# Kernel optimization log

Hardware: AMD Instinct MI355X
Metric: run time of the kernel (lower is better)

Reference implementation:

```python
import jax, jax.numpy as jnp
import numpy as np

N = 10000          # nodes
E = 320000         # edges
C = 128            # num_features (channels per irrep)
RB = 8             # radial basis size
NS = 10            # num_species
HID = 64           # radial MLP hidden
NPATH = 5          # TP paths: 0x0->0, 0x1->1, 1x0->1, 1x1->0(dot), 1x1->1(cross)
EPS = 0.17677669529663687  # 1/sqrt(avg_degree=32)


def setup_inputs() -> dict:
    key = jax.random.key(0)
    ks = jax.random.split(key, 20)
    inp = {
        "vectors": jax.random.normal(ks[0], (E, 3), jnp.float32),
        "node_feats": jax.random.normal(ks[1], (N, C * 4), jnp.float32),
        "node_specie": jax.random.randint(ks[2], (N,), 0, NS),
        "radial_embedding": jax.random.normal(ks[3], (E, RB), jnp.float32),
        "senders": jax.random.randint(ks[4], (E,), 0, N),
        "receivers": jax.random.randint(ks[5], (E,), 0, N),
    }
    s = 1.0 / np.sqrt(C)
    inp["W_up_s"] = jax.random.normal(ks[6], (C, C), jnp.float32) * s
    inp["W_up_v"] = jax.random.normal(ks[7], (C, C), jnp.float32) * s
    inp["W_rad1"] = jax.random.normal(ks[8], (RB, HID), jnp.float32) / np.sqrt(RB)
    inp["W_rad2"] = jax.random.normal(ks[9], (HID, NPATH * C), jnp.float32) / np.sqrt(HID)
    inp["W_down_s"] = jax.random.normal(ks[10], (C, C), jnp.float32) * s
    inp["W_down_v"] = jax.random.normal(ks[11], (C, C), jnp.float32) * s
    inp["W_skip_s"] = jax.random.normal(ks[12], (NS, C, C), jnp.float32) * s
    inp["W_skip_v"] = jax.random.normal(ks[13], (NS, C, C), jnp.float32) * s
    inp["W_prod_s"] = jax.random.normal(ks[14], (NS, 3, C), jnp.float32)
    inp["W_prod_v"] = jax.random.normal(ks[15], (NS, 2, C), jnp.float32)
    inp["W_lin_s"] = jax.random.normal(ks[16], (C, C), jnp.float32) * s
    inp["W_lin_v"] = jax.random.normal(ks[17], (C, C), jnp.float32) * s
    inp["W_ro"] = jax.random.normal(ks[18], (C, 1), jnp.float32) * s
    return inp


def _mace_forward(vectors, node_feats, node_specie, radial_embedding, senders,
                  receivers, W_up_s, W_up_v, W_rad1, W_rad2, W_down_s, W_down_v,
                  W_skip_s, W_skip_v, W_prod_s, W_prod_v, W_lin_s, W_lin_v, W_ro):
    n = node_feats.shape[0]
    # split flat mul_ir layout: [C x 0e | C x 1o]
    s = node_feats[:, :C]                      # [N, C]
    v = node_feats[:, C:].reshape(n, C, 3)     # [N, C, 3]

    # --- skip connection (species-indexed linear, first=False) ---
    Ws = W_skip_s[node_specie]                 # [N, C, C]
    Wv = W_skip_v[node_specie]
    sc_s = jnp.einsum('nc,ncd->nd', s, Ws)
    sc_v = jnp.einsum('nci,ncd->ndi', v, Wv)

    # --- interaction: linear_up ---
    h_s = s @ W_up_s
    h_v = jnp.einsum('nci,cd->ndi', v, W_up_v)

    # spherical harmonics (component normalization): Y1 = sqrt(3)*r_hat
    norm = jnp.linalg.norm(vectors, axis=-1, keepdims=True)
    Y1 = jnp.sqrt(3.0) * vectors / (norm + 1e-9)           # [E, 3]

    # radial MLP -> per-edge, per-path, per-channel TP weights
    w = jax.nn.silu(radial_embedding @ W_rad1) @ W_rad2
    w = w.reshape(-1, NPATH, C)                            # [E, 5, C]

    # gather sender features, depthwise ('uvu') CG tensor product with Y
    s_j = h_s[senders]                                     # [E, C]
    v_j = h_v[senders]                                     # [E, C, 3]
    dot = jnp.einsum('eci,ei->ec', v_j, Y1)                # 1o x 1o -> 0e
    crs = jnp.cross(v_j, Y1[:, None, :])                   # 1o x 1o -> 1o
    m_s = w[:, 0] * s_j + w[:, 3] * dot                    # [E, C]
    m_v = (w[:, 1][:, :, None] * s_j[:, :, None] * Y1[:, None, :]
           + w[:, 2][:, :, None] * v_j
           + w[:, 4][:, :, None] * crs)                    # [E, C, 3]

    # scatter to receivers
    agg_s = jax.ops.segment_sum(m_s, receivers, num_segments=n)
    agg_v = jax.ops.segment_sum(m_v, receivers, num_segments=n)

    # linear_down + epsilon scaling
    f_s = (agg_s @ W_down_s) * EPS
    f_v = jnp.einsum('nci,cd->ndi', agg_v, W_down_v) * EPS

    # --- equivariant product basis (correlation=2, symmetric) ---
    # order-1 and order-2 symmetric contractions for (0e, 1o) inputs:
    # scalars: A_s, A_s^2, |A_v|^2 ; vectors: A_v, A_s * A_v
    B_s = jnp.stack([f_s, f_s * f_s, jnp.sum(f_v * f_v, axis=-1)], axis=1)  # [N,3,C]
    B_v = jnp.stack([f_v, f_s[:, :, None] * f_v], axis=1)                    # [N,2,C,3]
    p_s = jnp.einsum('nkc,nkc->nc', B_s, W_prod_s[node_specie])
    p_v = jnp.einsum('nkci,nkc->nci', B_v, W_prod_v[node_specie])
    out_s = p_s @ W_lin_s + sc_s
    out_v = jnp.einsum('nci,cd->ndi', p_v, W_lin_v) + sc_v

    # --- linear readout (not last layer): invariant 0e output ---
    node_outputs = out_s @ W_ro                            # [N, 1]
    new_feats = jnp.concatenate([out_s, out_v.reshape(n, C * 3)], axis=-1)
    return node_outputs, new_feats


def reference(vectors, node_feats, node_specie, radial_embedding, senders,
              receivers, W_up_s, W_up_v, W_rad1, W_rad2, W_down_s, W_down_v,
              W_skip_s, W_skip_v, W_prod_s, W_prod_v, W_lin_s, W_lin_v, W_ro):
    return _mace_forward(vectors, node_feats, node_specie, radial_embedding,
                         senders, receivers, W_up_s, W_up_v, W_rad1, W_rad2,
                         W_down_s, W_down_v, W_skip_s, W_skip_v, W_prod_s,
                         W_prod_v, W_lin_s, W_lin_v, W_ro)
```

## Files before the change

### kernel.cpp

```cpp
#include <hip/hip_runtime.h>
#include <hip/hip_bf16.h>


#define NN 10000
#define EE 320000
#define FEPS 0.17677669529663687f

typedef __attribute__((ext_vector_type(4))) float f32x4;
typedef __attribute__((ext_vector_type(8))) short s16x8;

__device__ __forceinline__ float bflo(unsigned u) { return __uint_as_float(u << 16); }
__device__ __forceinline__ float bfhi(unsigned u) { return __uint_as_float(u & 0xffff0000u); }
__device__ __forceinline__ unsigned short f2bu(float f) {
    unsigned u = __float_as_uint(f);
    return (unsigned short)((u + 0x7FFFu + ((u >> 16) & 1u)) >> 16);
}
__device__ __forceinline__ unsigned pack2(float a, float b) {
    return (unsigned)f2bu(a) | ((unsigned)f2bu(b) << 16);
}
__device__ __forceinline__ s16x8 pack8(float4 a, float4 b) {
    union { s16x8 v; unsigned short u[8]; } r;
    r.u[0] = f2bu(a.x); r.u[1] = f2bu(a.y); r.u[2] = f2bu(a.z); r.u[3] = f2bu(a.w);
    r.u[4] = f2bu(b.x); r.u[5] = f2bu(b.y); r.u[6] = f2bu(b.z); r.u[7] = f2bu(b.w);
    return r.v;
}

#define TWN (26 * 16384)
#define W2N (640 * 64)
#define PREPX 20
#define HISTB 1250
__global__ __launch_bounds__(256) void k_prep_hist(
    const float* __restrict__ Wus, const float* __restrict__ Wuv,
    const float* __restrict__ Wds, const float* __restrict__ Wdv,
    const float* __restrict__ Wls, const float* __restrict__ Wlv,
    const float* __restrict__ Wss, const float* __restrict__ Wsv,
    const float* __restrict__ W_rad2,
    unsigned short* __restrict__ T,
    unsigned short* __restrict__ w2t,
    const int* __restrict__ recv, int* __restrict__ cnt) {
    const int b = blockIdx.x, tid = threadIdx.x;
    if (b < 26) {
        __shared__ unsigned short tr[128][130];
        const int m = b;
        const float* src;
        if (m == 0) src = Wus; else if (m == 1) src = Wuv;
        else if (m == 2) src = Wds; else if (m == 3) src = Wdv;
        else if (m == 4) src = Wls; else if (m == 5) src = Wlv;
        else if (m < 16) src = Wss + (size_t)(m - 6) * 16384;
        else src = Wsv + (size_t)(m - 16) * 16384;
        for (int i = tid; i < 16384; i += 256) {
            const int c = i >> 7, d = i & 127;
            tr[d][c] = f2bu(src[i]);
        }
        __syncthreads();
        unsigned* o32 = (unsigned*)(T + (size_t)m * 16384);
        for (int i = tid; i < 8192; i += 256) {
            const int d = i >> 6, c2 = (i & 63) * 2;
            o32[i] = (unsigned)tr[d][c2] | ((unsigned)tr[d][c2 + 1] << 16);
        }
    } else if (b < 26 + PREPX) {
        for (int i = (b - 26) * 256 + tid; i < W2N; i += PREPX * 256) {
            const int n = i >> 6, k = i & 63;
            w2t[i] = f2bu(W_rad2[k * 640 + n]);
        }
    } else {
        const int e = (b - (26 + PREPX)) * 256 + tid;
        if (e < EE) {
            int r = recv[e];
            r = ((unsigned)r < NN) ? r : 0;
            atomicAdd(&cnt[r], 1);
        }
    }
}

__global__ __launch_bounds__(1024) void k_scan_spec(
    const int* __restrict__ cnt, int* __restrict__ offs, int* __restrict__ cur,
    const int* __restrict__ specie, int* __restrict__ perm,
    int2* __restrict__ tiles, int* __restrict__ ntiles) {
    __shared__ int sums[1024];
    __shared__ int hcnt[10], hbase[10], hcur[10], tbase[11];
    const int t = threadIdx.x;
    const int chunk = (NN + 1023) / 1024;
    const int start = t * chunk;
    int local = 0;
    for (int i = 0; i < chunk; i++) {
        int idx = start + i;
        if (idx < NN) local += cnt[idx];
    }
    sums[t] = local;
    __syncthreads();
    for (int ofs = 1; ofs < 1024; ofs <<= 1) {
        int u = (t >= ofs) ? sums[t - ofs] : 0;
        __syncthreads();
        sums[t] += u;
        __syncthreads();
    }
    int base = (t == 0) ? 0 : sums[t - 1];
    for (int i = 0; i < chunk; i++) {
        int idx = start + i;
        if (idx < NN) {
            offs[idx] = base;
            cur[idx] = base;
            base += cnt[idx];
        }
    }
    if (t == 0) offs[NN] = sums[1023];
    if (t < 10) hcnt[t] = 0;
    __syncthreads();
    for (int n = t; n < NN; n += 1024) {
        int s = specie[n];
        s = ((unsigned)s < 10) ? s : 0;
        atomicAdd(&hcnt[s], 1);
    }
    __syncthreads();
    if (t == 0) {
        int run = 0, tc = 0;
        for (int sp = 0; sp < 10; sp++) {
            hbase[sp] = run; hcur[sp] = run; run += hcnt[sp];
            tbase[sp] = tc;  tc += (hcnt[sp] + 15) >> 4;
        }
        tbase[10] = tc;
        *ntiles = tc;
    }
    __syncthreads();
    const int tc = tbase[10];
    for (int ti = t; ti < tc; ti += 1024) {
        int sp = 0;
        while (sp < 9 && ti >= tbase[sp + 1]) sp++;
        const int b = (ti - tbase[sp]) * 16;
        tiles[ti] = make_int2(hbase[sp] + b, (sp << 8) | min(16, hcnt[sp] - b));
    }
    for (int n = t; n < NN; n += 1024) {
        int s = specie[n];
        s = ((unsigned)s < 10) ? s : 0;
        int slot = atomicAdd(&hcur[s], 1);
        if ((unsigned)slot < NN) perm[slot] = n;
    }
}

__global__ __launch_bounds__(256) void k_fill_pre(
    const int* __restrict__ recv, int* __restrict__ cur, int* __restrict__ csr,
    const float* __restrict__ nf,
    const unsigned short* __restrict__ Tw,
    uint2* __restrict__ h4o,
    const int* __restrict__ perm, const int2* __restrict__ tiles,
    const int* __restrict__ ntiles,
    float4* __restrict__ sc4) {
    if (blockIdx.x >= 640) {
        const int e = (blockIdx.x - 640) * 256 + threadIdx.x;
        if (e < EE) {
            int r = recv[e];
            r = ((unsigned)r < NN) ? r : 0;
            int slot = atomicAdd(&cur[r], 1);
            if ((unsigned)slot < EE) csr[slot] = e;
        }
        return;
    }
    const int tile = blockIdx.x;
    if (tile >= *ntiles) return;
    const int2 td = tiles[tile];
    const int base = td.x, sp = td.y >> 8, cnt16 = td.y & 255;
    __shared__ int nodesl[16];
    __shared__ float nfl[16][512];
    const int tid = threadIdx.x;
    if (tid < 16) nodesl[tid] = perm[base + ((tid < cnt16) ? tid : 0)];
    __syncthreads();
    {
        float4* dst = (float4*)nfl;
        for (int i = tid; i < 2048; i += 256) {
            const int r = i >> 7, off = i & 127;
            dst[i] = ((const float4*)(nf + (size_t)nodesl[r] * 512))[off];
        }
    }
    __syncthreads();
    const int lane = tid & 63, wv = tid >> 6;
    const int col = lane & 15, quad = lane >> 4;
    const float* rp = nfl[col];
    s16x8 Af[4][4];
#pragma unroll
    for (int kt = 0; kt < 4; kt++) {
        const int ko = kt * 32 + quad * 8;
        const float4 fa = *(const float4*)(rp + ko);
        const float4 fb = *(const float4*)(rp + ko + 4);
        Af[0][kt] = pack8(fa, fb);
#pragma unroll
        for (int i = 0; i < 3; i++) {
            union { s16x8 v; unsigned short u[8]; } A;
#pragma unroll
            for (int j = 0; j < 8; j++) A.u[j] = f2bu(rp[128 + 3 * (ko + j) + i]);
            Af[1 + i][kt] = A.v;
        }
    }
    const unsigned short* Ts = Tw;
    const unsigned short* Tv = Tw + 16384;
    const unsigned short* Tss = Tw + (size_t)(6 + sp) * 16384;
    const unsigned short* Tsv = Tw + (size_t)(16 + sp) * 16384;
#pragma unroll
    for (int nt = 0; nt < 2; nt++) {
        const int d = 32 * wv + 16 * nt + col;
        f32x4 C[4];
#pragma unroll
        for (int m = 0; m < 4; m++) C[m] = (f32x4){0.f, 0.f, 0.f, 0.f};
#pragma unroll
        for (int kt = 0; kt < 4; kt++) {
            const int ko = kt * 32 + quad * 8;
            const s16x8 Bs = *(const s16x8*)&Ts[(size_t)d * 128 + ko];
            const s16x8 Bv = *(const s16x8*)&Tv[(size_t)d * 128 + ko];
            C[0] = __builtin_amdgcn_mfma_f32_16x16x32_bf16(Af[0][kt], Bs, C[0], 0, 0, 0);
#pragma unroll
            for (int i = 0; i < 3; i++)
                C[1 + i] = __builtin_amdgcn_mfma_f32_16x16x32_bf16(Af[1 + i][kt], Bv, C[1 + i], 0, 0, 0);
        }
        const int P = ((d >> 5) << 4) + (d & 15);
        const int half = (d >> 4) & 1;
#pragma unroll
        for (int reg = 0; reg < 4; reg++) {
            const int node = nodesl[quad * 4 + reg];
            h4o[((size_t)node * 64 + P) * 2 + half] =
                make_uint2(pack2(C[0][reg], C[1][reg]), pack2(C[2][reg], C[3][reg]));
        }
        f32x4 CS[4];
#pragma unroll
        for (int m = 0; m < 4; m++) CS[m] = (f32x4){0.f, 0.f, 0.f, 0.f};
#pragma unroll
        for (int kt = 0; kt < 4; kt++) {
            const int ko = kt * 32 + quad * 8;
            const s16x8 Bss = *(const s16x8*)&Tss[(size_t)d * 128 + ko];
            const s16x8 Bsv = *(const s16x8*)&Tsv[(size_t)d * 128 + ko];
            CS[0] = __builtin_amdgcn_mfma_f32_16x16x32_bf16(Af[0][kt], Bss, CS[0], 0, 0, 0);
#pragma unroll
            for (int i = 0; i < 3; i++)
                CS[1 + i] = __builtin_amdgcn_mfma_f32_16x16x32_bf16(Af[1 + i][kt], Bsv, CS[1 + i], 0, 0, 0);
        }
#pragma unroll
        for (int reg = 0; reg < 4; reg++) {
            const int node = nodesl[quad * 4 + reg];
            sc4[(size_t)node * 128 + d] =
                make_float4(CS[0][reg], CS[1][reg], CS[2][reg], CS[3][reg]);
        }
    }
}

#define EGRID 2560
__global__ __launch_bounds__(256, 2) void k_edge_mfma(
    const float* __restrict__ vectors,
    const float* __restrict__ radial,
    const int* __restrict__ senders,
    const float* __restrict__ W_rad1,
    const unsigned short* __restrict__ w2t,
    const uint4* __restrict__ h4q,
    const int* __restrict__ offs, const int* __restrict__ csr,
    unsigned short* __restrict__ aggb) {
    __shared__ unsigned short w1s[512];
    __shared__ float4 em[3][64];
    __shared__ float radl[3][64][8];
    __shared__ unsigned short hidb[2 * 64 * 72];
    const int tid = threadIdx.x;
    const int lane = tid & 63, wv = tid >> 6;
    const int row = lane & 15, quad = lane >> 4;
    const int sE = tid >> 2, st = tid & 3;
    for (int i = tid; i < 512; i += 256) w1s[i] = f2bu(W_rad1[i]);

    s16x8 Bf[2][5][2];
#pragma unroll
    for (int ti = 0; ti < 2; ti++) {
        const int t = 2 * wv + ti;
#pragma unroll
        for (int p = 0; p < 5; p++) {
            const unsigned short* bp =
                w2t + (size_t)(128 * p + 16 * t + row) * 64 + quad * 8;
            Bf[ti][p][0] = *(const s16x8*)(bp);
            Bf[ti][p][1] = *(const s16x8*)(bp + 32);
        }
    }

    int curN = blockIdx.x, curS = offs[curN], curD = offs[curN + 1] - curS, curC0 = 0;
    int nxtN = curN, nxtS = curS, nxtD = curD, nxtC0 = 0;
    {
        nxtC0 += 64;
        if (nxtC0 >= nxtD) {
            nxtN += EGRID;
            if (nxtN < NN) { nxtS = offs[nxtN]; nxtD = offs[nxtN + 1] - nxtS; }
            nxtC0 = 0;
        }
    }
    int nx2N = nxtN, nx2S = nxtS, nx2D = nxtD, nx2C0 = nxtC0;
    if (nx2N < NN) {
        nx2C0 += 64;
        if (nx2C0 >= nx2D) {
            nx2N += EGRID;
            if (nx2N < NN) { nx2S = offs[nx2N]; nx2D = offs[nx2N + 1] - nx2S; }
            nx2C0 = 0;
        }
    }

    if (st < 2) {
        const int gi = curC0 + sE;
        if (gi < curD) {
            int e = csr[curS + gi];
            e = ((unsigned)e < EE) ? e : 0;
            if (st == 0) {
                int j = senders[e];
                j = ((unsigned)j < NN) ? j : 0;
                const float vx = vectors[e * 3 + 0];
                const float vy = vectors[e * 3 + 1];
                const float vz = vectors[e * 3 + 2];
                const float inr = 1.7320508075688772f /
                    (sqrtf(vx * vx + vy * vy + vz * vz) + 1e-9f);
                em[0][sE] = make_float4(__int_as_float(j), vx * inr, vy * inr, vz * inr);
            } else {
                *(float4*)&radl[0][sE][0] = *(const float4*)(radial + (size_t)e * 8);
                *(float4*)&radl[0][sE][4] = *(const float4*)(radial + (size_t)e * 8 + 4);
            }
        } else {
            if (st == 0) em[0][sE] = make_float4(0.f, 0.f, 0.f, 0.f);
            else {
                *(float4*)&radl[0][sE][0] = make_float4(0.f, 0.f, 0.f, 0.f);
                *(float4*)&radl[0][sE][4] = make_float4(0.f, 0.f, 0.f, 0.f);
            }
        }
    }
    int eReg = -1;
    if (nxtN < NN && st < 2) {
        const int gi = nxtC0 + sE;
        if (gi < nxtD) {
            int e = csr[nxtS + gi];
            eReg = ((unsigned)e < EE) ? e : 0;
        }
    }
    __syncthreads();

    float acc_s[2] = {0.f, 0.f}, av0[2] = {0.f, 0.f},
          av1[2] = {0.f, 0.f}, av2[2] = {0.f, 0.f};
    int cs = 0, hbI = 0;
    while (true) {
        const int ws = (cs == 2) ? 0 : cs + 1;
        const bool hasNxt = (nxtN < NN);
        const float4* emc = em[cs];
        const float* emf = (const float*)emc;
        uint4 hqA[4];
#pragma unroll
        for (int rg = 0; rg < 4; rg++) {
            const int j = __float_as_int(emf[(quad * 4 + rg) * 4]);
            hqA[rg] = h4q[(size_t)j * 64 + (wv << 4) + row];
        }
        bool sv = false;
        float4 ra0 = make_float4(0.f, 0.f, 0.f, 0.f);
        float4 ra1 = make_float4(0.f, 0.f, 0.f, 0.f);
        if (hasNxt && st < 2 && eReg >= 0) {
            sv = true;
            const int e = eReg;
            if (st == 0) {
                int j = senders[e];
                j = ((unsigned)j < NN) ? j : 0;
                ra0 = make_float4(vectors[e * 3 + 0], vectors[e * 3 + 1],
                                  vectors[e * 3 + 2], __int_as_float(j));
            } else {
                ra0 = *(const float4*)(radial + (size_t)e * 8);
                ra1 = *(const float4*)(radial + (size_t)e * 8 + 4);
            }
        }
        int eRegN = -1;
        if (nx2N < NN && st < 2) {
            const int gi = nx2C0 + sE;
            if (gi < nx2D) {
                int e = csr[nx2S + gi];
                eRegN = ((unsigned)e < EE) ? e : 0;
            }
        }
        const int glimC = min(64, curD - curC0);
        {
            const int g16C = (glimC + 15) & ~15;
            unsigned short* hb = hidb + hbI * 4608;
            const int u0 = st * 16;
            if (sE < glimC) {
                float rr[8];
                *(float4*)&rr[0] = *(const float4*)&radl[cs][sE][0];
                *(float4*)&rr[4] = *(const float4*)&radl[cs][sE][4];
#pragma unroll
                for (int h = 0; h < 2; h++) {
                    float a[8];
#pragma unroll
                    for (int u = 0; u < 8; u++) a[u] = 0.f;
#pragma unroll
                    for (int r = 0; r < 8; r++) {
                        const uint4 wa = *(const uint4*)&w1s[r * 64 + u0 + h * 8];
                        const float f = rr[r];
                        a[0] += f * bflo(wa.x); a[1] += f * bfhi(wa.x);
                        a[2] += f * bflo(wa.y); a[3] += f * bfhi(wa.y);
                        a[4] += f * bflo(wa.z); a[5] += f * bfhi(wa.z);
                        a[6] += f * bflo(wa.w); a[7] += f * bfhi(wa.w);
                    }
                    unsigned o[4];
#pragma unroll
                    for (int k = 0; k < 4; k++) {
                        const float s0 = a[2 * k] / (1.f + __expf(-a[2 * k]));
                        const float s1 = a[2 * k + 1] / (1.f + __expf(-a[2 * k + 1]));
                        o[k] = pack2(s0, s1);
                    }
                    *(uint4*)&hb[sE * 72 + u0 + h * 8] = make_uint4(o[0], o[1], o[2], o[3]);
                }
            } else if (sE < g16C) {
                *(uint4*)&hb[sE * 72 + u0] = make_uint4(0, 0, 0, 0);
                *(uint4*)&hb[sE * 72 + u0 + 8] = make_uint4(0, 0, 0, 0);
            }
        }
        if (hasNxt && st < 2) {
            if (st == 0) {
                if (sv) {
                    const float vx = ra0.x, vy = ra0.y, vz = ra0.z;
                    const float inr = 1.7320508075688772f /
                        (sqrtf(vx * vx + vy * vy + vz * vz) + 1e-9f);
                    em[ws][sE] = make_float4(ra0.w, vx * inr, vy * inr, vz * inr);
                } else {
                    em[ws][sE] = make_float4(0.f, 0.f, 0.f, 0.f);
                }
            } else {
                *(float4*)&radl[ws][sE][0] = ra0;
                *(float4*)&radl[ws][sE][4] = ra1;
            }
        }
        __syncthreads();
        {
            __builtin_amdgcn_s_setprio(1);
            const unsigned short* hb = hidb + hbI * 4608;
            for (int g0 = 0; g0 < glimC; g0 += 16) {
                const s16x8 A0 = *(const s16x8*)&hb[(g0 + row) * 72 + quad * 8];
                const s16x8 A1 = *(const s16x8*)&hb[(g0 + row) * 72 + 32 + quad * 8];
                float4 mm[4];
#pragma unroll
                for (int rg = 0; rg < 4; rg++) mm[rg] = emc[g0 + quad * 4 + rg];
                const bool more = (g0 + 16) < glimC;
                uint4 hqB[4];
                if (more) {
#pragma unroll
                    for (int rg = 0; rg < 4; rg++) {
                        const int j = __float_as_int(emf[(g0 + 16 + quad * 4 + rg) * 4]);
                        hqB[rg] = h4q[(size_t)j * 64 + (wv << 4) + row];
                    }
                }
#pragma unroll
                for (int ti = 0; ti < 2; ti++) {
                    float sj[4], a0r[4], a1r[4], a2r[4];
#pragma unroll
                    for (int rg = 0; rg < 4; rg++) {
                        const unsigned wx = ti ? hqA[rg].z : hqA[rg].x;
                        const unsigned wy = ti ? hqA[rg].w : hqA[rg].y;
                        sj[rg] = bflo(wx); a0r[rg] = bfhi(wx);
                        a1r[rg] = bflo(wy); a2r[rg] = bfhi(wy);
                    }
#pragma unroll
                    for (int p = 0; p < 5; p++) {
                        f32x4 z = {0.f, 0.f, 0.f, 0.f};
                        z = __builtin_amdgcn_mfma_f32_16x16x32_bf16(A0, Bf[ti][p][0], z, 0, 0, 0);
                        z = __builtin_amdgcn_mfma_f32_16x16x32_bf16(A1, Bf[ti][p][1], z, 0, 0, 0);
#pragma unroll
                        for (int rg = 0; rg < 4; rg++) {
                            const float w = z[rg];
                            const float y0 = mm[rg].y, y1 = mm[rg].z, y2 = mm[rg].w;
                            if (p == 0) {
                                acc_s[ti] += w * sj[rg];
                            } else if (p == 1) {
                                const float wsj = w * sj[rg];
                                av0[ti] += wsj * y0;
                                av1[ti] += wsj * y1;
                                av2[ti] += wsj * y2;
                            } else if (p == 2) {
                                av0[ti] += w * a0r[rg];
                                av1[ti] += w * a1r[rg];
                                av2[ti] += w * a2r[rg];
                            } else if (p == 3) {
                                acc_s[ti] += w * (a0r[rg] * y0 + a1r[rg] * y1 +
                                                  a2r[rg] * y2);
                            } else {
                                av0[ti] += w * (a1r[rg] * y2 - a2r[rg] * y1);
                                av1[ti] += w * (a2r[rg] * y0 - a0r[rg] * y2);
                                av2[ti] += w * (a0r[rg] * y1 - a1r[rg] * y0);
                            }
                        }
                    }
                }
                if (more) {
#pragma unroll
                    for (int rg = 0; rg < 4; rg++) hqA[rg] = hqB[rg];
                }
            }
            __builtin_amdgcn_s_setprio(0);
            if (curC0 + 64 >= curD) {
#pragma unroll
                for (int ti = 0; ti < 2; ti++) {
                    acc_s[ti] += __shfl_xor(acc_s[ti], 16); acc_s[ti] += __shfl_xor(acc_s[ti], 32);
                    av0[ti] += __shfl_xor(av0[ti], 16);     av0[ti] += __shfl_xor(av0[ti], 32);
                    av1[ti] += __shfl_xor(av1[ti], 16);     av1[ti] += __shfl_xor(av1[ti], 32);
                    av2[ti] += __shfl_xor(av2[ti], 16);     av2[ti] += __shfl_xor(av2[ti], 32);
                }
                if (lane < 16) {
                    unsigned short* og = aggb + (size_t)curN * 512;
#pragma unroll
                    for (int ti = 0; ti < 2; ti++) {
                        const int cc = 16 * (2 * wv + ti) + lane;
                        og[cc] = f2bu(acc_s[ti]);
                        og[128 + cc] = f2bu(av0[ti]);
                        og[256 + cc] = f2bu(av1[ti]);
                        og[384 + cc] = f2bu(av2[ti]);
                    }
                }
                acc_s[0] = acc_s[1] = 0.f; av0[0] = av0[1] = 0.f;
                av1[0] = av1[1] = 0.f;     av2[0] = av2[1] = 0.f;
            }
        }
        if (!hasNxt) break;
        curN = nxtN; curS = nxtS; curD = nxtD; curC0 = nxtC0;
        nxtN = nx2N; nxtS = nx2S; nxtD = nx2D; nxtC0 = nx2C0;
        if (nx2N < NN) {
            nx2C0 += 64;
            if (nx2C0 >= nx2D) {
                nx2N += EGRID;
                if (nx2N < NN) { nx2S = offs[nx2N]; nx2D = offs[nx2N + 1] - nx2S; }
                nx2C0 = 0;
            }
        }
        eReg = eRegN;
        cs = ws; hbI ^= 1;
    }
}

__global__ __launch_bounds__(256) void k_post_mfma(
    const unsigned short* __restrict__ aggb,
    const int* __restrict__ perm,
    const int2* __restrict__ tiles,
    const int* __restrict__ ntiles,
    const unsigned short* __restrict__ Tw,
    const float* __restrict__ Wps,
    const float* __restrict__ Wpv,
    const float* __restrict__ Wro,
    const float4* __restrict__ sc4,
    float* __restrict__ dout) {
    const int tile = blockIdx.x;
    if (tile >= *ntiles) return;
    const int2 td = tiles[tile];
    const int base = td.x, sp = td.y >> 8, cnt = td.y & 255;
    __shared__ int nodesl[16];
    __shared__ float rol[16];
    __shared__ unsigned short Pl[4][16][128];
    const int tid = threadIdx.x;
    if (tid < 16) {
        nodesl[tid] = perm[base + ((tid < cnt) ? tid : 0)];
        rol[tid] = 0.f;
    }
    __syncthreads();
    const int lane = tid & 63, wv = tid >> 6;
    const int col = lane & 15, quad = lane >> 4;
    const int aN = nodesl[col];
    const unsigned short* Tds = Tw + (size_t)2 * 16384;
    const unsigned short* Tdv = Tw + (size_t)3 * 16384;
    const unsigned short* Tls = Tw + (size_t)4 * 16384;
    const unsigned short* Tlv = Tw + (size_t)5 * 16384;
#pragma unroll
    for (int nt = 0; nt < 2; nt++) {
        const int d = 32 * wv + 16 * nt + col;
        f32x4 CF[4];
#pragma unroll
        for (int m = 0; m < 4; m++) CF[m] = (f32x4){0.f, 0.f, 0.f, 0.f};
#pragma unroll
        for (int kt = 0; kt < 4; kt++) {
            const int ko = kt * 32 + quad * 8;
            const s16x8 Bs = *(const s16x8*)&Tds[(size_t)d * 128 + ko];
            const s16x8 Bv = *(const s16x8*)&Tdv[(size_t)d * 128 + ko];
#pragma unroll
            for (int m = 0; m < 4; m++) {
                const s16x8 A = *(const s16x8*)&aggb[(size_t)aN * 512 + m * 128 + ko];
                CF[m] = __builtin_amdgcn_mfma_f32_16x16x32_bf16(A, m ? Bv : Bs, CF[m], 0, 0, 0);
            }
        }
        const float wps0 = Wps[sp * 384 + d];
        const float wps1 = Wps[sp * 384 + 128 + d];
        const float wps2 = Wps[sp * 384 + 256 + d];
        const float wpv0 = Wpv[sp * 256 + d];
        const float wpv1 = Wpv[sp * 256 + 128 + d];
#pragma unroll
        for (int reg = 0; reg < 4; reg++) {
            const float fs = CF[0][reg] * FEPS;
            const float f0 = CF[1][reg] * FEPS;
            const float f1 = CF[2][reg] * FEPS;
            const float f2 = CF[3][reg] * FEPS;
            const float ps = fs * wps0 + fs * fs * wps1 + (f0 * f0 + f1 * f1 + f2 * f2) * wps2;
            const float pb = wpv0 + fs * wpv1;
            const int r = quad * 4 + reg;
            Pl[0][r][d] = f2bu(ps);
            Pl[1][r][d] = f2bu(f0 * pb);
            Pl[2][r][d] = f2bu(f1 * pb);
            Pl[3][r][d] = f2bu(f2 * pb);
        }
    }
    __syncthreads();
#pragma unroll
    for (int nt = 0; nt < 2; nt++) {
        const int d = 32 * wv + 16 * nt + col;
        f32x4 CL[4];
#pragma unroll
        for (int m = 0; m < 4; m++) CL[m] = (f32x4){0.f, 0.f, 0.f, 0.f};
#pragma unroll
        for (int kt = 0; kt < 4; kt++) {
            const int ko = kt * 32 + quad * 8;
            const s16x8 Bls = *(const s16x8*)&Tls[(size_t)d * 128 + ko];
            const s16x8 Blv = *(const s16x8*)&Tlv[(size_t)d * 128 + ko];
#pragma unroll
            for (int m = 0; m < 4; m++) {
                const s16x8 A = *(const s16x8*)&Pl[m][col][ko];
                CL[m] = __builtin_amdgcn_mfma_f32_16x16x32_bf16(A, m ? Blv : Bls, CL[m], 0, 0, 0);
            }
        }
        const float wro = Wro[d];
#pragma unroll
        for (int reg = 0; reg < 4; reg++) {
            const int r = quad * 4 + reg;
            if (r < cnt) {
                const int node = nodesl[r];
                const float4 scv = sc4[(size_t)node * 128 + d];
                const float outs = CL[0][reg] + scv.x;
                const float o0 = CL[1][reg] + scv.y;
                const float o1 = CL[2][reg] + scv.z;
                const float o2 = CL[3][reg] + scv.w;
                float* o = dout + NN + (size_t)node * 512;
                o[d] = outs;
                o[128 + 3 * d + 0] = o0;
                o[128 + 3 * d + 1] = o1;
                o[128 + 3 * d + 2] = o2;
                atomicAdd(&rol[r], outs * wro);
            }
        }
    }
    __syncthreads();
    if (tid < 16 && tid < cnt) dout[nodesl[tid]] = rol[tid];
}

extern "C" void kernel_launch(void* const* d_in, const int* in_sizes, int n_in,
                              void* d_out, int out_size, void* d_ws, size_t ws_size,
                              hipStream_t stream) {
    const float* vectors    = (const float*)d_in[0];
    const float* node_feats = (const float*)d_in[1];
    const int*   specie     = (const int*)d_in[2];
    const float* radial     = (const float*)d_in[3];
    const int*   senders    = (const int*)d_in[4];
    const int*   receivers  = (const int*)d_in[5];
    const float* W_up_s     = (const float*)d_in[6];
    const float* W_up_v     = (const float*)d_in[7];
    const float* W_rad1     = (const float*)d_in[8];
    const float* W_rad2     = (const float*)d_in[9];
    const float* W_down_s   = (const float*)d_in[10];
    const float* W_down_v   = (const float*)d_in[11];
    const float* W_skip_s   = (const float*)d_in[12];
    const float* W_skip_v   = (const float*)d_in[13];
    const float* W_prod_s   = (const float*)d_in[14];
    const float* W_prod_v   = (const float*)d_in[15];
    const float* W_lin_s    = (const float*)d_in[16];
    const float* W_lin_v    = (const float*)d_in[17];
    const float* W_ro       = (const float*)d_in[18];
    float* out = (float*)d_out;

    char* w = (char*)d_ws;
    auto align256 = [](size_t x) { return (x + 255) & ~(size_t)255; };
    int* cnt  = (int*)w;              w += align256((size_t)NN * 4);
    int* offs = (int*)w;              w += align256((size_t)(NN + 1) * 4);
    int* cur  = (int*)w;              w += align256((size_t)NN * 4);
    int* csr  = (int*)w;              w += align256((size_t)EE * 4);
    uint4* h4q = (uint4*)w;           w += align256((size_t)NN * 64 * 16);
    unsigned short* aggb = (unsigned short*)w;  w += align256((size_t)NN * 512 * 2);
    unsigned short* w2t  = (unsigned short*)w;  w += align256((size_t)W2N * 2);
    unsigned short* Tw   = (unsigned short*)w;  w += align256((size_t)TWN * 2);
    int* perm   = (int*)w;            w += align256((size_t)NN * 4);
    int2* tiles = (int2*)w;           w += align256((size_t)640 * 8);
    int* ntiles = (int*)w;            w += align256(4);
    float4* sc4 = (float4*)w;         w += align256((size_t)NN * 128 * 16);

    hipMemsetAsync(cnt, 0, (size_t)NN * 4, stream);
    k_prep_hist<<<26 + PREPX + HISTB, 256, 0, stream>>>(
        W_up_s, W_up_v, W_down_s, W_down_v, W_lin_s, W_lin_v,
        W_skip_s, W_skip_v, W_rad2, Tw, w2t, receivers, cnt);
    k_scan_spec<<<1, 1024, 0, stream>>>(cnt, offs, cur, specie, perm, tiles, ntiles);
    k_fill_pre<<<640 + HISTB, 256, 0, stream>>>(
        receivers, cur, csr, node_feats, Tw, (uint2*)h4q,
        perm, tiles, ntiles, sc4);
    k_edge_mfma<<<EGRID, 256, 0, stream>>>(vectors, radial, senders, W_rad1,
                                           w2t, h4q, offs, csr, aggb);
    k_post_mfma<<<640, 256, 0, stream>>>(aggb, perm, tiles, ntiles,
                                         Tw, W_prod_s, W_prod_v, W_ro, sc4, out);
}
```

Baseline: 356.5 us.

## Store skip buffer as bf16, pad shared arrays, shrink edge grid

```diff
diff --git a/kernel.cpp b/kernel.cpp
--- a/kernel.cpp
+++ b/kernel.cpp
@@ -145,7 +145,7 @@
     uint2* __restrict__ h4o,
     const int* __restrict__ perm, const int2* __restrict__ tiles,
     const int* __restrict__ ntiles,
-    float4* __restrict__ sc4) {
+    uint2* __restrict__ scb) {
     if (blockIdx.x >= 640) {
         const int e = (blockIdx.x - 640) * 256 + threadIdx.x;
         if (e < EE) {
@@ -161,15 +161,15 @@
     const int2 td = tiles[tile];
     const int base = td.x, sp = td.y >> 8, cnt16 = td.y & 255;
     __shared__ int nodesl[16];
-    __shared__ float nfl[16][512];
+    __shared__ float nfl[16][516];
     const int tid = threadIdx.x;
     if (tid < 16) nodesl[tid] = perm[base + ((tid < cnt16) ? tid : 0)];
     __syncthreads();
     {
-        float4* dst = (float4*)nfl;
         for (int i = tid; i < 2048; i += 256) {
-            const int r = i >> 7, off = i & 127;
-            dst[i] = ((const float4*)(nf + (size_t)nodesl[r] * 512))[off];
+            const int r = i >> 7, off4 = (i & 127) * 4;
+            *(float4*)&nfl[r][off4] =
+                ((const float4*)(nf + (size_t)nodesl[r] * 512))[i & 127];
         }
     }
     __syncthreads();
@@ -235,13 +235,13 @@
 #pragma unroll
         for (int reg = 0; reg < 4; reg++) {
             const int node = nodesl[quad * 4 + reg];
-            sc4[(size_t)node * 128 + d] =
-                make_float4(CS[0][reg], CS[1][reg], CS[2][reg], CS[3][reg]);
-        }
-    }
-}
-
-#define EGRID 2560
+            scb[(size_t)node * 128 + d] =
+                make_uint2(pack2(CS[0][reg], CS[1][reg]), pack2(CS[2][reg], CS[3][reg]));
+        }
+    }
+}
+
+#define EGRID 1024
 __global__ __launch_bounds__(256, 2) void k_edge_mfma(
     const float* __restrict__ vectors,
     const float* __restrict__ radial,
@@ -534,7 +534,7 @@
     const float* __restrict__ Wps,
     const float* __restrict__ Wpv,
     const float* __restrict__ Wro,
-    const float4* __restrict__ sc4,
+    const uint2* __restrict__ scb,
     float* __restrict__ dout) {
     const int tile = blockIdx.x;
     if (tile >= *ntiles) return;
@@ -542,7 +542,7 @@
     const int base = td.x, sp = td.y >> 8, cnt = td.y & 255;
     __shared__ int nodesl[16];
     __shared__ float rol[16];
-    __shared__ unsigned short Pl[4][16][128];
+    __shared__ unsigned short Pl[4][16][136];
     const int tid = threadIdx.x;
     if (tid < 16) {
         nodesl[tid] = perm[base + ((tid < cnt) ? tid : 0)];
@@ -617,11 +617,11 @@
             const int r = quad * 4 + reg;
             if (r < cnt) {
                 const int node = nodesl[r];
-                const float4 scv = sc4[(size_t)node * 128 + d];
-                const float outs = CL[0][reg] + scv.x;
-                const float o0 = CL[1][reg] + scv.y;
-                const float o1 = CL[2][reg] + scv.z;
-                const float o2 = CL[3][reg] + scv.w;
+                const uint2 sv = scb[(size_t)node * 128 + d];
+                const float outs = CL[0][reg] + bflo(sv.x);
+                const float o0 = CL[1][reg] + bfhi(sv.x);
+                const float o1 = CL[2][reg] + bflo(sv.y);
+                const float o2 = CL[3][reg] + bfhi(sv.y);
                 float* o = dout + NN + (size_t)node * 512;
                 o[d] = outs;
                 o[128 + 3 * d + 0] = o0;
@@ -672,7 +672,7 @@
     int* perm   = (int*)w;            w += align256((size_t)NN * 4);
     int2* tiles = (int2*)w;           w += align256((size_t)640 * 8);
     int* ntiles = (int*)w;            w += align256(4);
-    float4* sc4 = (float4*)w;         w += align256((size_t)NN * 128 * 16);
+    uint2* scb  = (uint2*)w;          w += align256((size_t)NN * 128 * 8);
 
     hipMemsetAsync(cnt, 0, (size_t)NN * 4, stream);
     k_prep_hist<<<26 + PREPX + HISTB, 256, 0, stream>>>(
@@ -681,9 +681,9 @@
     k_scan_spec<<<1, 1024, 0, stream>>>(cnt, offs, cur, specie, perm, tiles, ntiles);
     k_fill_pre<<<640 + HISTB, 256, 0, stream>>>(
         receivers, cur, csr, node_feats, Tw, (uint2*)h4q,
-        perm, tiles, ntiles, sc4);
+        perm, tiles, ntiles, scb);
     k_edge_mfma<<<EGRID, 256, 0, stream>>>(vectors, radial, senders, W_rad1,
                                            w2t, h4q, offs, csr, aggb);
     k_post_mfma<<<640, 256, 0, stream>>>(aggb, perm, tiles, ntiles,
-                                         Tw, W_prod_s, W_prod_v, W_ro, sc4, out);
-}
+                                         Tw, W_prod_s, W_prod_v, W_ro, scb, out);
+}
```

Result: faster. 339.8 us (-4.7%).
